# Optimization experiments

Hardware: AMD Instinct MI355X
Metric: run time of the kernel (lower is better)

Reference implementation:

```python
import jax, jax.numpy as jnp
import numpy as np

H = 32      # query heads
KV = 8      # kv heads
D = 128     # head_dim
HID = 4096
S = 4       # num sequences
L = 1024    # tokens per sequence
N = S * L   # total tokens
EPS = 1e-6
THETA = 10000.0
GROUPS = H // KV


def setup_inputs() -> dict:
    key = jax.random.key(0)
    ks = jax.random.split(key, 12)
    def w(k, shape, std):
        return jax.random.normal(k, shape, dtype=jnp.float32) * std
    return {
        "hidden": w(ks[0], (N, HID), 1.0),
        "mu_prev": w(ks[1], (N, HID), 1.0),
        "positions": jnp.tile(jnp.arange(L, dtype=jnp.int32), S),
        "Wq": w(ks[2], (H * D, HID), HID ** -0.5),
        "Wk": w(ks[3], (KV * D, HID), HID ** -0.5),
        "Wv": w(ks[4], (KV * D, HID), HID ** -0.5),
        "Wo": w(ks[5], (HID, H * D), (H * D) ** -0.5),
        "Wmq": w(ks[6], (H * D, HID), 0.01),
        "Wmk": w(ks[7], (KV * D, HID), 0.01),
        "Wmv": w(ks[8], (KV * D, HID), 0.01),
        "q_norm_w": jnp.ones((D,), jnp.float32),
        "k_norm_w": jnp.ones((D,), jnp.float32),
    }


def _rmsnorm(x, w):
    var = jnp.mean(jnp.square(x), axis=-1, keepdims=True)
    return x * jax.lax.rsqrt(var + EPS) * w


def _rope_cos_sin(positions):
    inv_freq = 1.0 / (THETA ** (jnp.arange(0, D, 2, dtype=jnp.float32) / D))  # [D/2]
    freqs = positions.astype(jnp.float32)[:, None] * inv_freq[None, :]        # [N, D/2]
    emb = jnp.concatenate([freqs, freqs], axis=-1)                            # [N, D]
    return jnp.cos(emb), jnp.sin(emb)


def _rotate_half(x):
    x1, x2 = jnp.split(x, 2, axis=-1)
    return jnp.concatenate([-x2, x1], axis=-1)


def _apply_rotary(x, cos, sin):
    # x: [N, h, D]; cos/sin: [N, D]
    return x * cos[:, None, :] + _rotate_half(x) * sin[:, None, :]


def reference(hidden, mu_prev, positions, Wq, Wk, Wv, Wo, Wmq, Wmk, Wmv, q_norm_w, k_norm_w):
    # QKV projections + mu-bias fusion
    q = hidden @ Wq.T + mu_prev @ Wmq.T     # [N, H*D]
    k = hidden @ Wk.T + mu_prev @ Wmk.T     # [N, KV*D]
    v = hidden @ Wv.T + mu_prev @ Wmv.T     # [N, KV*D]
    q = q.reshape(N, H, D)
    k = k.reshape(N, KV, D)
    v = v.reshape(N, KV, D)
    # QK RMSNorm
    q = _rmsnorm(q, q_norm_w)
    k = _rmsnorm(k, k_norm_w)
    # RoPE
    cos, sin = _rope_cos_sin(positions)
    q = _apply_rotary(q, cos, sin)
    k = _apply_rotary(k, cos, sin)
    # GQA: expand kv heads to match q heads
    k = jnp.repeat(k, GROUPS, axis=1)       # [N, H, D]
    v = jnp.repeat(v, GROUPS, axis=1)
    # Varlen causal attention: equal-length seqs -> batched [S, L, H, D]
    qs = q.reshape(S, L, H, D)
    ks = k.reshape(S, L, H, D)
    vs = v.reshape(S, L, H, D)
    scale = 1.0 / np.sqrt(D)
    scores = jnp.einsum("slhd,smhd->shlm", qs, ks) * scale   # [S, H, L, L]
    causal = jnp.tril(jnp.ones((L, L), dtype=bool))
    scores = jnp.where(causal, scores, jnp.finfo(scores.dtype).min)
    probs = jax.nn.softmax(scores, axis=-1)
    out = jnp.einsum("shlm,smhd->slhd", probs, vs)           # [S, L, H, D]
    out = out.reshape(N, H * D)
    return out @ Wo.T                                         # [N, HID]
```

## Files before the change

### kernel.cpp

```cpp
#include <hip/hip_runtime.h>
#include <hip/hip_bf16.h>
#include <stdint.h>

#define DEV static __device__ __forceinline__

typedef __bf16 bf16_t;
typedef __bf16 bf16x8 __attribute__((ext_vector_type(8)));
typedef __bf16 bf16x4 __attribute__((ext_vector_type(4)));
typedef __bf16 bf16x2 __attribute__((ext_vector_type(2)));
typedef float  f32x4  __attribute__((ext_vector_type(4)));


DEV void gload_lds16(const void* g, void* l) {
  __builtin_amdgcn_global_load_lds(
      (__attribute__((address_space(1))) void*)(uintptr_t)(g),
      (__attribute__((address_space(3))) void*)(uintptr_t)(l),
      16, 0, 0);
}

#define BARRIER() asm volatile("s_barrier" ::: "memory")
#define MFMA16(a, b, c) __builtin_amdgcn_mfma_f32_16x16x32_bf16((a), (b), (c), 0, 0, 0)

DEV void pack_pair_chunk8(const float* __restrict__ A, const float* __restrict__ B,
                          bf16_t* __restrict__ dst, size_t i) {
  size_t r = i >> 9, c = i & 511;
  const float4* pa = (const float4*)A + r * 1024 + c * 2;
  const float4* pb = (const float4*)B + r * 1024 + c * 2;
  float4 a0 = pa[0], a1 = pa[1];
  float4 b0 = pb[0], b1 = pb[1];
  bf16x8 oa = {(bf16_t)a0.x, (bf16_t)a0.y, (bf16_t)a0.z, (bf16_t)a0.w,
               (bf16_t)a1.x, (bf16_t)a1.y, (bf16_t)a1.z, (bf16_t)a1.w};
  bf16x8 ob = {(bf16_t)b0.x, (bf16_t)b0.y, (bf16_t)b0.z, (bf16_t)b0.w,
               (bf16_t)b1.x, (bf16_t)b1.y, (bf16_t)b1.z, (bf16_t)b1.w};
  ((bf16x8*)dst)[r * 1024 + c]       = oa;
  ((bf16x8*)dst)[r * 1024 + 512 + c] = ob;
}

__global__ void k_pack_all(const float* __restrict__ hidden, const float* __restrict__ mu,
                           const float* __restrict__ Wq, const float* __restrict__ Wmq,
                           const float* __restrict__ Wk, const float* __restrict__ Wmk,
                           const float* __restrict__ Wv, const float* __restrict__ Wmv,
                           const float* __restrict__ Wo,
                           bf16_t* __restrict__ Xb, bf16_t* __restrict__ Wqkv,
                           bf16_t* __restrict__ Wob) {
  const size_t t0 = 2097152, t1 = 4194304, t2 = 4718592, t3 = 5242880, t4 = 7340032;
  size_t stride = (size_t)gridDim.x * blockDim.x;
  for (size_t i = (size_t)blockIdx.x * blockDim.x + threadIdx.x; i < t4; i += stride) {
    if (i < t0) {
      pack_pair_chunk8(hidden, mu, Xb, i);
    } else if (i < t1) {
      pack_pair_chunk8(Wq, Wmq, Wqkv, i - t0);
    } else if (i < t2) {
      pack_pair_chunk8(Wk, Wmk, Wqkv + (size_t)4096 * 8192, i - t1);
    } else if (i < t3) {
      pack_pair_chunk8(Wv, Wmv, Wqkv + (size_t)5120 * 8192, i - t2);
    } else {
      size_t j = i - t3;
      const float4* p = (const float4*)Wo + j * 2;
      float4 v0 = p[0], v1 = p[1];
      bf16x8 o = {(bf16_t)v0.x, (bf16_t)v0.y, (bf16_t)v0.z, (bf16_t)v0.w,
                  (bf16_t)v1.x, (bf16_t)v1.y, (bf16_t)v1.z, (bf16_t)v1.w};
      ((bf16x8*)Wob)[j] = o;
    }
  }
}

template<typename CT, int NSPLIT>
__global__ __launch_bounds__(512, 2) void k_gemm256(
    const bf16_t* __restrict__ A, const bf16_t* __restrict__ B,
    CT* __restrict__ C, int M, int N, int Kfull) {
  __shared__ __align__(16) char lds[131072];
  const int tid = threadIdx.x, lane = tid & 63, wid = tid >> 6;
  const int l15 = lane & 15, lhi = lane >> 4;
  const int wr = wid >> 2, wc = wid & 3;
  const int bid = blockIdx.x, nwg = gridDim.x;
  const int cpx = nwg >> 3;
  const int swz = (bid & 7) * cpx + (bid >> 3);
  const int nbm = M >> 8;
  const int tiles = nbm * (N >> 8);
  const int ks = (NSPLIT > 1) ? (swz / tiles) : 0;
  const int t  = (NSPLIT > 1) ? (swz % tiles) : swz;
  const int bm = t % nbm, bn = t / nbm;
  const int Kloop = Kfull / NSPLIT;
  const int nkt = Kloop >> 6;

  const size_t rowK = (size_t)Kfull * 2;
  const size_t kbase = (size_t)ks * Kloop * 2;
  const int off0 = wid * 1024 + lane * 16, off1 = off0 + 8192;
  const int r0 = off0 >> 7, r1 = off1 >> 7;
  const int c0 = ((off0 >> 4) & 7) ^ (r0 & 7);
  const int c1 = ((off1 >> 4) & 7) ^ (r1 & 7);
  const char* sA0 = (const char*)A + ((size_t)bm * 256 + r0) * rowK + kbase + c0 * 16;
  const char* sA1 = (const char*)A + ((size_t)bm * 256 + r1) * rowK + kbase + c1 * 16;
  const char* sB0 = (const char*)B + ((size_t)bn * 256 + r0) * rowK + kbase + c0 * 16;
  const char* sB1 = (const char*)B + ((size_t)bn * 256 + r1) * rowK + kbase + c1 * 16;
  const size_t hst = (size_t)128 * rowK;

  enum { A0S = 0, A1S = 16384, A2S = 32768, A3S = 49152,
         B0S = 65536, B1S = 81920, B2S = 98304, B3S = 114688 };

#define STG(slot, pa, pb, off) do { \
    gload_lds16((pa) + (off), lds + (slot) + wid * 1024); \
    gload_lds16((pb) + (off), lds + (slot) + 8192 + wid * 1024); } while (0)

  const bf16_t* Ae = (const bf16_t*)(lds + A0S + wr * 16384);
  const bf16_t* Be = (const bf16_t*)(lds + B0S + (wc >> 1) * 16384);
  const bf16_t* Ao = (const bf16_t*)(lds + A2S + wr * 16384);
  const bf16_t* Bo = (const bf16_t*)(lds + B2S + (wc >> 1) * 16384);
  const int bro = (wc & 1) * 64;

  f32x4 acc[8][4] = {};
  bf16x8 a[4][2], b[4][2];
  const int xr = l15 & 7;
  const int ck0 = (lhi ^ xr) * 8;
  const int ck1 = ((4 + lhi) ^ xr) * 8;

#define RD_A(base, rb) do { _Pragma("unroll") \
    for (int mi = 0; mi < 4; ++mi) { \
      const int ro = ((rb) + mi * 16 + l15) * 64; \
      a[mi][0] = *(const bf16x8*)((base) + ro + ck0); \
      a[mi][1] = *(const bf16x8*)((base) + ro + ck1); } } while (0)
#define RD_B2(base, n0) do { _Pragma("unroll") \
    for (int n = (n0); n < (n0) + 2; ++n) { \
      const int ro = (bro + n * 16 + l15) * 64; \
      b[n][0] = *(const bf16x8*)((base) + ro + ck0); \
      b[n][1] = *(const bf16x8*)((base) + ro + ck1); } } while (0)
#define MM(qm, qn) do { _Pragma("unroll") \
    for (int mi = 0; mi < 4; ++mi) { _Pragma("unroll") \
      for (int ni = 0; ni < 2; ++ni) { \
        f32x4 t_ = acc[(qm) * 4 + mi][(qn) * 2 + ni]; \
        t_ = MFMA16(a[mi][0], b[(qn) * 2 + ni][0], t_); \
        t_ = MFMA16(a[mi][1], b[(qn) * 2 + ni][1], t_); \
        acc[(qm) * 4 + mi][(qn) * 2 + ni] = t_; } } } while (0)
#define PRIO_MM(qm, qn) do { __builtin_amdgcn_s_setprio(1); MM(qm, qn); \
    __builtin_amdgcn_s_setprio(0); } while (0)

  STG(B0S, sB0, sB1, 0);
  STG(B1S, sB0, sB1, hst);
  STG(A0S, sA0, sA1, 0);
  STG(A1S, sA0, sA1, hst);
  STG(B2S, sB0, sB1, 128);
  STG(B3S, sB0, sB1, 128 + hst);
  STG(A2S, sA0, sA1, 128);
  asm volatile("s_waitcnt vmcnt(6)" ::: "memory");
  BARRIER();

  size_t g = 0;
  for (int ktp = 0; ktp < nkt / 2 - 1; ++ktp) {
    RD_A(Ae, 0); RD_B2(Be, 0);
    STG(A3S, sA0, sA1, g + 128 + hst);
    BARRIER();
    STG(B0S, sB0, sB1, g + 256);
    RD_B2(Be, 2);
    PRIO_MM(0, 0);
    BARRIER();
    PRIO_MM(0, 1);
    BARRIER();
    RD_A(Ae, 64);
    STG(B1S, sB0, sB1, g + 256 + hst);
    BARRIER();
    PRIO_MM(1, 0);
    BARRIER();
    STG(A0S, sA0, sA1, g + 256);
    BARRIER();
    PRIO_MM(1, 1);
    asm volatile("s_waitcnt vmcnt(6)" ::: "memory");
    BARRIER();
    RD_A(Ao, 0); RD_B2(Bo, 0);
    STG(A1S, sA0, sA1, g + 256 + hst);
    BARRIER();
    STG(B2S, sB0, sB1, g + 384);
    RD_B2(Bo, 2);
    PRIO_MM(0, 0);
    BARRIER();
    PRIO_MM(0, 1);
    BARRIER();
    RD_A(Ao, 64);
    STG(B3S, sB0, sB1, g + 384 + hst);
    BARRIER();
    PRIO_MM(1, 0);
    BARRIER();
    STG(A2S, sA0, sA1, g + 384);
    BARRIER();
    PRIO_MM(1, 1);
    asm volatile("s_waitcnt vmcnt(6)" ::: "memory");
    BARRIER();
    g += 256;
  }
  RD_A(Ae, 0); RD_B2(Be, 0); RD_B2(Be, 2);
  STG(A3S, sA0, sA1, g + 128 + hst);
  BARRIER();
  PRIO_MM(0, 0);
  PRIO_MM(0, 1);
  RD_A(Ae, 64);
  PRIO_MM(1, 0);
  PRIO_MM(1, 1);
  asm volatile("s_waitcnt vmcnt(0)" ::: "memory");
  BARRIER();
  RD_A(Ao, 0); RD_B2(Bo, 0); RD_B2(Bo, 2);
  PRIO_MM(0, 0);
  PRIO_MM(0, 1);
  RD_A(Ao, 64);
  PRIO_MM(1, 0);
  PRIO_MM(1, 1);

  CT* Cp = C + (size_t)ks * M * N;
#pragma unroll
  for (int m = 0; m < 8; ++m) {
    const int row0 = bm * 256 + wr * 128 + m * 16 + 4 * lhi;
#pragma unroll
    for (int n = 0; n < 4; ++n) {
      const int col = bn * 256 + wc * 64 + n * 16 + l15;
#pragma unroll
      for (int i = 0; i < 4; ++i)
        Cp[(size_t)(row0 + i) * N + col] = (CT)acc[m][n][i];
    }
  }
#undef STG
#undef RD_A
#undef RD_B2
#undef MM
#undef PRIO_MM
}

__global__ __launch_bounds__(256) void k_norm_rope(
    const bf16_t* __restrict__ qkvA, const bf16_t* __restrict__ qkvB,
    const int* __restrict__ pos,
    const float* __restrict__ qw, const float* __restrict__ kw,
    bf16_t* __restrict__ Q, bf16_t* __restrict__ Kk, bf16_t* __restrict__ V) {
  const int lane = threadIdx.x & 63, wid = threadIdx.x >> 6;
  const int l32 = lane & 31;
  const int gslot = blockIdx.x * 8 + wid * 2 + (lane >> 5);
  const int n = gslot / 48, slot = gslot % 48;
  const int d0 = 2 * l32;
  const bf16_t* rowA = qkvA + (size_t)n * 6144;
  const bf16_t* rowB = qkvB + (size_t)n * 6144;

  if (slot >= 40) {
    const int h2 = slot - 40;
    const int c = 5120 + h2 * 128 + d0;
    bf16x2 aL = *(const bf16x2*)(rowA + c),     bL = *(const bf16x2*)(rowB + c);
    bf16x2 aH = *(const bf16x2*)(rowA + c + 64), bH = *(const bf16x2*)(rowB + c + 64);
    bf16x2 oL = {(bf16_t)((float)aL[0] + (float)bL[0]), (bf16_t)((float)aL[1] + (float)bL[1])};
    bf16x2 oH = {(bf16_t)((float)aH[0] + (float)bH[0]), (bf16_t)((float)aH[1] + (float)bH[1])};
    bf16_t* dst = V + ((size_t)n * 8 + h2) * 128;
    *(bf16x2*)(dst + d0) = oL;
    *(bf16x2*)(dst + d0 + 64) = oH;
    return;
  }
  const bool isq = slot < 32;
  const int h = isq ? slot : slot - 32;
  const int c = (isq ? h * 128 : 4096 + h * 128) + d0;
  bf16x2 aL = *(const bf16x2*)(rowA + c),      bL = *(const bf16x2*)(rowB + c);
  bf16x2 aH = *(const bf16x2*)(rowA + c + 64), bH = *(const bf16x2*)(rowB + c + 64);
  float xL0 = (float)aL[0] + (float)bL[0], xL1 = (float)aL[1] + (float)bL[1];
  float xH0 = (float)aH[0] + (float)bH[0], xH1 = (float)aH[1] + (float)bH[1];
  float ss = xL0 * xL0 + xL1 * xL1 + xH0 * xH0 + xH1 * xH1;
#pragma unroll
  for (int m = 16; m; m >>= 1) ss += __shfl_xor(ss, m, 64);
  const float inv = rsqrtf(ss * (1.0f / 128.0f) + 1e-6f);
  const float* wgt = isq ? qw : kw;
  float yL0 = xL0 * inv * wgt[d0],      yL1 = xL1 * inv * wgt[d0 + 1];
  float yH0 = xH0 * inv * wgt[d0 + 64], yH1 = xH1 * inv * wgt[d0 + 65];
  const float p = (float)pos[n];
  const float ang0 = p * expf((float)d0 * -0.14391156608f);
  const float ang1 = p * expf((float)(d0 + 1) * -0.14391156608f);
  float s0, c0f, s1, c1f;
  sincosf(ang0, &s0, &c0f);
  sincosf(ang1, &s1, &c1f);
  bf16x2 oL = {(bf16_t)(yL0 * c0f - yH0 * s0), (bf16_t)(yL1 * c1f - yH1 * s1)};
  bf16x2 oH = {(bf16_t)(yH0 * c0f + yL0 * s0), (bf16_t)(yH1 * c1f + yL1 * s1)};
  bf16_t* dst = isq ? (Q + ((size_t)n * 32 + h) * 128) : (Kk + ((size_t)n * 8 + h) * 128);
  *(bf16x2*)(dst + d0) = oL;
  *(bf16x2*)(dst + d0 + 64) = oH;
}

__global__ __launch_bounds__(256) void k_vt(const bf16_t* __restrict__ V,
                                            bf16_t* __restrict__ Vt) {
  __shared__ bf16_t T[64][136];
  const int blk = blockIdx.x;
  const int tt = blk & 15, kvh = (blk >> 4) & 7, s = blk >> 7;
  const int tok0 = tt * 64;
  const int tid = threadIdx.x;
#pragma unroll
  for (int k = 0; k < 4; ++k) {
    const int item = tid + k * 256;
    const int tok = item >> 4, d0 = (item & 15) * 8;
    bf16x8 v = *(const bf16x8*)(V + ((size_t)(s * 1024 + tok0 + tok) * 8 + kvh) * 128 + d0);
    *(bf16x8*)(&T[tok][d0]) = v;
  }
  __syncthreads();
#pragma unroll
  for (int k = 0; k < 4; ++k) {
    const int item = tid + k * 256;
    const int d = item & 127, oct = item >> 7;
    bf16x8 o;
#pragma unroll
    for (int j = 0; j < 8; ++j) o[j] = T[oct * 8 + j][d];
    *(bf16x8*)(Vt + ((size_t)((s * 8 + kvh) * 128 + d)) * 1024 + tok0 + oct * 8) = o;
  }
}

__global__ __launch_bounds__(256, 2) void k_attn(
    const bf16_t* __restrict__ Q, const bf16_t* __restrict__ Kk,
    const bf16_t* __restrict__ Vt, bf16_t* __restrict__ O) {
  __shared__ __align__(16) bf16_t Ks[2][64 * 128];
  __shared__ __align__(16) bf16_t Ps[4][32 * 72];
  const int b = blockIdx.x;
  const int x = b & 7, y = b >> 3;
  const int h = x * 4 + ((y >> 3) & 3);
  const int qb = 7 - (y & 7);
  const int s = y >> 5;
  const int kvh = h >> 2;
  const int tid = threadIdx.x, lane = tid & 63, wid = tid >> 6;
  const int l15 = lane & 15, lhi = lane >> 4;

  bf16x8 qf[2][4];
  {
    const int qrow = qb * 128 + wid * 32;
#pragma unroll
    for (int mt = 0; mt < 2; mt++) {
      const size_t base = ((size_t)(s * 1024 + qrow + mt * 16 + l15) * 32 + h) * 128;
#pragma unroll
      for (int kc = 0; kc < 4; kc++)
        qf[mt][kc] = *(const bf16x8*)(Q + base + kc * 32 + 8 * lhi);
    }
  }
  const bf16_t* Vtb = Vt + (size_t)((s * 8 + kvh) * 128) * 1024;

  f32x4 of[2][8] = {};
  float mx[2][4], li[2][4];
#pragma unroll
  for (int mt = 0; mt < 2; mt++)
#pragma unroll
    for (int i = 0; i < 4; i++) { mx[mt][i] = -1e30f; li[mt][i] = 0.f; }

  const int ktiles = (qb + 1) * 2;

  const int so = wid * 4096;
#define STAGE_K(kt_, buf_) do { _Pragma("unroll") \
    for (int c = 0; c < 4; ++c) { \
      const int o = so + c * 1024 + lane * 16; \
      const int krow = o >> 8; \
      const int cs = ((o >> 4) & 15) ^ (krow & 7); \
      const char* src = (const char*)(Kk + \
          ((size_t)(s * 1024 + (kt_) * 64 + krow) * 8 + kvh) * 128) + cs * 16; \
      gload_lds16(src, (char*)&Ks[buf_][0] + so + c * 1024); \
    } } while (0)

  STAGE_K(0, 0);
  asm volatile("s_waitcnt vmcnt(0)" ::: "memory");
  BARRIER();

  for (int kt = 0; kt < ktiles; kt++) {
    const int kv0 = kt * 64;
    const int buf = kt & 1;
    if (kt + 1 < ktiles) STAGE_K(kt + 1, buf ^ 1);

    f32x4 sf[2][4] = {};
#pragma unroll
    for (int kc = 0; kc < 4; kc++) {
      bf16x8 kf[4];
#pragma unroll
      for (int n = 0; n < 4; n++) {
        const int krow = n * 16 + l15;
        const int ci = (kc * 4 + lhi) ^ (krow & 7);
        kf[n] = *(const bf16x8*)(&Ks[buf][0] + krow * 128 + ci * 8);
      }
#pragma unroll
      for (int mt = 0; mt < 2; mt++)
#pragma unroll
        for (int n = 0; n < 4; n++)
          sf[mt][n] = MFMA16(qf[mt][kc], kf[n], sf[mt][n]);
    }

    const bool masked = (kt >= 2 * qb);
    const float scale = 0.08838834764831845f;
    float pv[2][4][4];
#pragma unroll
    for (int mt = 0; mt < 2; mt++) {
#pragma unroll
      for (int i = 0; i < 4; i++) {
        float rm = -1e30f;
#pragma unroll
        for (int n = 0; n < 4; n++) {
          float sv = sf[mt][n][i] * scale;
          if (masked) {
            const int kvg = kv0 + n * 16 + l15;
            const int qg = qb * 128 + wid * 32 + mt * 16 + 4 * lhi + i;
            if (kvg > qg) sv = -1e30f;
          }
          pv[mt][n][i] = sv;
          rm = fmaxf(rm, sv);
        }
#pragma unroll
        for (int mm = 1; mm < 16; mm <<= 1) rm = fmaxf(rm, __shfl_xor(rm, mm, 64));
        const float nm = fmaxf(mx[mt][i], rm);
        float ts = 0.f;
#pragma unroll
        for (int n = 0; n < 4; n++) {
          float e = __expf(pv[mt][n][i] - nm);
          pv[mt][n][i] = e;
          ts += e;
        }
#pragma unroll
        for (int mm = 1; mm < 16; mm <<= 1) ts += __shfl_xor(ts, mm, 64);
        const float al = __expf(mx[mt][i] - nm);
        li[mt][i] = li[mt][i] * al + ts;
        mx[mt][i] = nm;
#pragma unroll
        for (int n = 0; n < 8; n++) of[mt][n][i] *= al;
      }
    }

    bf16_t* myP = &Ps[wid][0];
#pragma unroll
    for (int mt = 0; mt < 2; mt++)
#pragma unroll
      for (int n = 0; n < 4; n++)
#pragma unroll
        for (int i = 0; i < 4; i++)
          myP[(mt * 16 + 4 * lhi + i) * 72 + n * 16 + l15] = (bf16_t)pv[mt][n][i];

#pragma unroll
    for (int kc = 0; kc < 2; kc++) {
      bf16x8 pf[2];
#pragma unroll
      for (int mt = 0; mt < 2; mt++)
        pf[mt] = *(const bf16x8*)(myP + (mt * 16 + l15) * 72 + kc * 32 + 8 * lhi);
#pragma unroll
      for (int n = 0; n < 8; n++) {
        const int d = n * 16 + l15;
        bf16x8 vf = *(const bf16x8*)(Vtb + (size_t)d * 1024 + kv0 + kc * 32 + 8 * lhi);
#pragma unroll
        for (int mt = 0; mt < 2; mt++)
          of[mt][n] = MFMA16(pf[mt], vf, of[mt][n]);
      }
    }

    if (kt + 1 < ktiles) {
      asm volatile("s_waitcnt vmcnt(0)" ::: "memory");
      BARRIER();
    }
  }
#undef STAGE_K

#pragma unroll
  for (int mt = 0; mt < 2; mt++) {
#pragma unroll
    for (int i = 0; i < 4; i++) {
      const float invl = 1.0f / li[mt][i];
      const int tokrow = qb * 128 + wid * 32 + mt * 16 + 4 * lhi + i;
      bf16_t* dst = O + (size_t)(s * 1024 + tokrow) * 4096 + h * 128;
#pragma unroll
      for (int n = 0; n < 8; n++)
        dst[n * 16 + l15] = (bf16_t)(of[mt][n][i] * invl);
    }
  }
}

extern "C" void kernel_launch(void* const* d_in, const int* in_sizes, int n_in,
                              void* d_out, int out_size, void* d_ws, size_t ws_size,
                              hipStream_t stream) {
  const float* hidden = (const float*)d_in[0];
  const float* mu     = (const float*)d_in[1];
  const int*   pos    = (const int*)d_in[2];
  const float* Wq  = (const float*)d_in[3];
  const float* Wk  = (const float*)d_in[4];
  const float* Wv  = (const float*)d_in[5];
  const float* Wo  = (const float*)d_in[6];
  const float* Wmq = (const float*)d_in[7];
  const float* Wmk = (const float*)d_in[8];
  const float* Wmv = (const float*)d_in[9];
  const float* qw  = (const float*)d_in[10];
  const float* kw  = (const float*)d_in[11];
  float* out = (float*)d_out;
  char* ws = (char*)d_ws;

  if (ws_size < 301989888u) return;

  bf16_t* Wqkv = (bf16_t*)(ws);
  bf16_t* Wob  = (bf16_t*)(ws + 100663296);
  bf16_t* Xb   = (bf16_t*)(ws + 134217728);
  bf16_t* Qb   = (bf16_t*)(ws + 134217728);
  bf16_t* Kb   = (bf16_t*)(ws + 167772160);
  bf16_t* Vb   = (bf16_t*)(ws + 176160768);
  bf16_t* VtG  = (bf16_t*)(ws + 184549376);
  bf16_t* qkvA = (bf16_t*)(ws + 201326592);
  bf16_t* qkvB = (bf16_t*)(ws + 251658240);
  bf16_t* Ob   = (bf16_t*)(ws + 201326592);

  k_pack_all<<<2048, 256, 0, stream>>>(hidden, mu, Wq, Wmq, Wk, Wmk, Wv, Wmv, Wo,
                                       Xb, Wqkv, Wob);
  k_gemm256<bf16_t, 2><<<768, 512, 0, stream>>>(Xb, Wqkv, qkvA, 4096, 6144, 8192);
  k_norm_rope<<<24576, 256, 0, stream>>>(qkvA, qkvB, pos, qw, kw, Qb, Kb, Vb);
  k_vt<<<512, 256, 0, stream>>>(Vb, VtG);
  k_attn<<<1024, 256, 0, stream>>>(Qb, Kb, VtG, Ob);
  k_gemm256<float, 1><<<256, 512, 0, stream>>>(Ob, Wob, out, 4096, 4096, 4096);
}
```

Baseline: 755.1 us.

## Replace hand-scheduled multi-slot GEMM pipeline with simple LDS double buffering

The 256x256 bf16 GEMM kernel's interleaved schedule is replaced. It used eight 16 KB LDS slots, half-tile staging and many barriers between MFMA quadrants. The new version stages a whole 64-wide K tile per iteration into one of two 64 KB buffers, with a 128-byte row layout and XOR swizzle, and uses one wait and one barrier per iteration. This simplifies the code and cuts barrier count, but prefetch depth drops to one tile and each iteration fully drains outstanding global loads, so load latency may be less hidden.

```diff
diff --git a/kernel.cpp b/kernel.cpp
--- a/kernel.cpp
+++ b/kernel.cpp
@@ -79,52 +79,41 @@
   const int nbm = M >> 8;
   const int tiles = nbm * (N >> 8);
   const int ks = (NSPLIT > 1) ? (swz / tiles) : 0;
-  const int t  = (NSPLIT > 1) ? (swz % tiles) : swz;
-  const int bm = t % nbm, bn = t / nbm;
+  const int t0i = (NSPLIT > 1) ? (swz % tiles) : swz;
+  const int bm = t0i % nbm, bn = t0i / nbm;
   const int Kloop = Kfull / NSPLIT;
   const int nkt = Kloop >> 6;
 
   const size_t rowK = (size_t)Kfull * 2;
   const size_t kbase = (size_t)ks * Kloop * 2;
-  const int off0 = wid * 1024 + lane * 16, off1 = off0 + 8192;
-  const int r0 = off0 >> 7, r1 = off1 >> 7;
-  const int c0 = ((off0 >> 4) & 7) ^ (r0 & 7);
-  const int c1 = ((off1 >> 4) & 7) ^ (r1 & 7);
-  const char* sA0 = (const char*)A + ((size_t)bm * 256 + r0) * rowK + kbase + c0 * 16;
-  const char* sA1 = (const char*)A + ((size_t)bm * 256 + r1) * rowK + kbase + c1 * 16;
-  const char* sB0 = (const char*)B + ((size_t)bn * 256 + r0) * rowK + kbase + c0 * 16;
-  const char* sB1 = (const char*)B + ((size_t)bn * 256 + r1) * rowK + kbase + c1 * 16;
-  const size_t hst = (size_t)128 * rowK;
-
-  enum { A0S = 0, A1S = 16384, A2S = 32768, A3S = 49152,
-         B0S = 65536, B1S = 81920, B2S = 98304, B3S = 114688 };
-
-#define STG(slot, pa, pb, off) do { \
-    gload_lds16((pa) + (off), lds + (slot) + wid * 1024); \
-    gload_lds16((pb) + (off), lds + (slot) + 8192 + wid * 1024); } while (0)
-
-  const bf16_t* Ae = (const bf16_t*)(lds + A0S + wr * 16384);
-  const bf16_t* Be = (const bf16_t*)(lds + B0S + (wc >> 1) * 16384);
-  const bf16_t* Ao = (const bf16_t*)(lds + A2S + wr * 16384);
-  const bf16_t* Bo = (const bf16_t*)(lds + B2S + (wc >> 1) * 16384);
-  const int bro = (wc & 1) * 64;
+  const int srow = tid >> 3;
+  const int scs = (tid & 7) ^ (srow & 7);
+  const char* sA = (const char*)A + ((size_t)bm * 256 + srow) * rowK + kbase + scs * 16;
+  const char* sB = (const char*)B + ((size_t)bn * 256 + srow) * rowK + kbase + scs * 16;
+  const size_t r64 = (size_t)64 * rowK;
+
+#define STG(bufp, kb) do { _Pragma("unroll") \
+    for (int j = 0; j < 4; ++j) { \
+      gload_lds16(sA + (size_t)j * r64 + (kb), (bufp) + j * 8192 + tid * 16); \
+      gload_lds16(sB + (size_t)j * r64 + (kb), (bufp) + 32768 + j * 8192 + tid * 16); \
+    } } while (0)
 
   f32x4 acc[8][4] = {};
   bf16x8 a[4][2], b[4][2];
   const int xr = l15 & 7;
-  const int ck0 = (lhi ^ xr) * 8;
-  const int ck1 = ((4 + lhi) ^ xr) * 8;
-
-#define RD_A(base, rb) do { _Pragma("unroll") \
+  const int ck0 = ((lhi ^ xr)) * 16;
+  const int ck1 = (((4 + lhi) ^ xr)) * 16;
+
+#define RD_A(bufp, rb) do { _Pragma("unroll") \
     for (int mi = 0; mi < 4; ++mi) { \
-      const int ro = ((rb) + mi * 16 + l15) * 64; \
-      a[mi][0] = *(const bf16x8*)((base) + ro + ck0); \
-      a[mi][1] = *(const bf16x8*)((base) + ro + ck1); } } while (0)
-#define RD_B2(base, n0) do { _Pragma("unroll") \
+      const char* rp = (bufp) + (wr * 128 + (rb) + mi * 16 + l15) * 128; \
+      a[mi][0] = *(const bf16x8*)(rp + ck0); \
+      a[mi][1] = *(const bf16x8*)(rp + ck1); } } while (0)
+#define RD_B2(bufp, n0) do { _Pragma("unroll") \
     for (int n = (n0); n < (n0) + 2; ++n) { \
-      const int ro = (bro + n * 16 + l15) * 64; \
-      b[n][0] = *(const bf16x8*)((base) + ro + ck0); \
-      b[n][1] = *(const bf16x8*)((base) + ro + ck1); } } while (0)
+      const char* rp = (bufp) + 32768 + (wc * 64 + n * 16 + l15) * 128; \
+      b[n][0] = *(const bf16x8*)(rp + ck0); \
+      b[n][1] = *(const bf16x8*)(rp + ck1); } } while (0)
 #define MM(qm, qn) do { _Pragma("unroll") \
     for (int mi = 0; mi < 4; ++mi) { _Pragma("unroll") \
       for (int ni = 0; ni < 2; ++ni) { \
@@ -135,74 +124,26 @@
 #define PRIO_MM(qm, qn) do { __builtin_amdgcn_s_setprio(1); MM(qm, qn); \
     __builtin_amdgcn_s_setprio(0); } while (0)
 
-  STG(B0S, sB0, sB1, 0);
-  STG(B1S, sB0, sB1, hst);
-  STG(A0S, sA0, sA1, 0);
-  STG(A1S, sA0, sA1, hst);
-  STG(B2S, sB0, sB1, 128);
-  STG(B3S, sB0, sB1, 128 + hst);
-  STG(A2S, sA0, sA1, 128);
-  asm volatile("s_waitcnt vmcnt(6)" ::: "memory");
-  BARRIER();
-
-  size_t g = 0;
-  for (int ktp = 0; ktp < nkt / 2 - 1; ++ktp) {
-    RD_A(Ae, 0); RD_B2(Be, 0);
-    STG(A3S, sA0, sA1, g + 128 + hst);
-    BARRIER();
-    STG(B0S, sB0, sB1, g + 256);
-    RD_B2(Be, 2);
-    PRIO_MM(0, 0);
-    BARRIER();
-    PRIO_MM(0, 1);
-    BARRIER();
-    RD_A(Ae, 64);
-    STG(B1S, sB0, sB1, g + 256 + hst);
-    BARRIER();
-    PRIO_MM(1, 0);
-    BARRIER();
-    STG(A0S, sA0, sA1, g + 256);
-    BARRIER();
-    PRIO_MM(1, 1);
-    asm volatile("s_waitcnt vmcnt(6)" ::: "memory");
-    BARRIER();
-    RD_A(Ao, 0); RD_B2(Bo, 0);
-    STG(A1S, sA0, sA1, g + 256 + hst);
-    BARRIER();
-    STG(B2S, sB0, sB1, g + 384);
-    RD_B2(Bo, 2);
-    PRIO_MM(0, 0);
-    BARRIER();
-    PRIO_MM(0, 1);
-    BARRIER();
-    RD_A(Ao, 64);
-    STG(B3S, sB0, sB1, g + 384 + hst);
-    BARRIER();
-    PRIO_MM(1, 0);
-    BARRIER();
-    STG(A2S, sA0, sA1, g + 384);
-    BARRIER();
-    PRIO_MM(1, 1);
-    asm volatile("s_waitcnt vmcnt(6)" ::: "memory");
-    BARRIER();
-    g += 256;
-  }
-  RD_A(Ae, 0); RD_B2(Be, 0); RD_B2(Be, 2);
-  STG(A3S, sA0, sA1, g + 128 + hst);
-  BARRIER();
-  PRIO_MM(0, 0);
-  PRIO_MM(0, 1);
-  RD_A(Ae, 64);
-  PRIO_MM(1, 0);
-  PRIO_MM(1, 1);
+  STG(lds, 0);
   asm volatile("s_waitcnt vmcnt(0)" ::: "memory");
   BARRIER();
-  RD_A(Ao, 0); RD_B2(Bo, 0); RD_B2(Bo, 2);
-  PRIO_MM(0, 0);
-  PRIO_MM(0, 1);
-  RD_A(Ao, 64);
-  PRIO_MM(1, 0);
-  PRIO_MM(1, 1);
+
+  int bufo = 0;
+  for (int t = 0; t < nkt; ++t) {
+    const char* bp = lds + bufo;
+    RD_A(bp, 0);
+    RD_B2(bp, 0);
+    RD_B2(bp, 2);
+    if (t + 1 < nkt) STG(lds + (bufo ^ 65536), (size_t)(t + 1) * 128);
+    PRIO_MM(0, 0);
+    PRIO_MM(0, 1);
+    RD_A(bp, 64);
+    PRIO_MM(1, 0);
+    PRIO_MM(1, 1);
+    asm volatile("s_waitcnt vmcnt(0)" ::: "memory");
+    BARRIER();
+    bufo ^= 65536;
+  }
 
   CT* Cp = C + (size_t)ks * M * N;
 #pragma unroll
```

Result: slower. 838.3 us (+11.0%).
